# Kernel optimization log

Measured on AMD Instinct MI355X. Metric: run time of the kernel, lower is better.

Reference implementation:

```python
import jax, jax.numpy as jnp
import numpy as np

N_NODES = 50000
N_EDGES = 800000
D = 64
E_DIM = 2
C = 8


def _spline_basis(pseudo, K):
    """Open B-spline basis, degree=1. pseudo: [Ne, E] in [0,1).
    Returns basis B [Ne, S] and flat weight index WI [Ne, S], S = 2**E."""
    E = pseudo.shape[1]
    v = pseudo * (K - 1)
    lo_f = jnp.floor(v)
    frac = v - lo_f
    lo = lo_f.astype(jnp.int32)
    idx = jnp.stack([jnp.clip(lo, 0, K - 1), jnp.clip(lo + 1, 0, K - 1)], axis=-1)  # [Ne,E,2]
    bas = jnp.stack([1.0 - frac, frac], axis=-1)                                   # [Ne,E,2]
    combos = jnp.asarray(
        np.stack(np.meshgrid(*([np.arange(2)] * E), indexing='ij'), -1).reshape(-1, E)
    )  # [S,E]
    d_idx = jnp.arange(E)[None, :]          # broadcast to [S,E]
    B = jnp.prod(bas[:, d_idx, combos], axis=-1)  # [Ne,S]
    stride = (K ** jnp.arange(E)).astype(jnp.int32)  # [E]
    WI = jnp.sum(idx[:, d_idx, combos] * stride[None, None, :], axis=-1)  # [Ne,S]
    return B, WI


def _spline_conv(x, src, dst, pseudo, W, root, bias, K, num_nodes):
    """SplineConv (degree=1, open spline, aggr='mean', root_weight, bias).
    x: [N,Din], W: [K**E, Din, Dout], root: [Din, Dout]."""
    B, WI = _spline_basis(pseudo, K)                 # [Ne,S], [Ne,S]
    Y = jnp.einsum('nd,kdo->nko', x, W)              # [N, K**E, Dout]
    gathered = Y[src[:, None], WI]                   # [Ne, S, Dout]
    m = jnp.einsum('es,eso->eo', B, gathered)        # [Ne, Dout]
    msum = jax.ops.segment_sum(m, dst, num_segments=num_nodes)
    cnt = jax.ops.segment_sum(jnp.ones((m.shape[0], 1), m.dtype), dst, num_segments=num_nodes)
    aggr = msum / jnp.maximum(cnt, 1.0)
    return aggr + x @ root + bias


def setup_inputs() -> dict:
    key = jax.random.key(0)
    ks = jax.random.split(key, 16)
    s = 1.0 / np.sqrt(D)
    return {
        'x': jax.random.normal(ks[0], (N_NODES, D), jnp.float32),
        'edge_index': jax.random.randint(ks[1], (2, N_EDGES), 0, N_NODES, jnp.int32),
        'edge_attr': jax.random.uniform(ks[2], (N_EDGES, E_DIM), jnp.float32),
        'W1': jax.random.normal(ks[3], (3 ** E_DIM, D, D), jnp.float32) * s,
        'root1': jax.random.normal(ks[4], (D, D), jnp.float32) * s,
        'b1': jax.random.normal(ks[5], (D,), jnp.float32) * 0.01,
        'W2': jax.random.normal(ks[6], (5 ** E_DIM, D, D), jnp.float32) * s,
        'root2': jax.random.normal(ks[7], (D, D), jnp.float32) * s,
        'b2': jax.random.normal(ks[8], (D,), jnp.float32) * 0.01,
        'mlp1_w': jax.random.normal(ks[9], (D, D), jnp.float32) * s,
        'mlp1_b': jax.random.normal(ks[10], (D,), jnp.float32) * 0.01,
        'mlp2_w': jax.random.normal(ks[11], (D, C), jnp.float32) * s,
        'mlp2_b': jax.random.normal(ks[12], (C,), jnp.float32) * 0.01,
    }


def reference(x, edge_index, edge_attr, W1, root1, b1, W2, root2, b2,
              mlp1_w, mlp1_b, mlp2_w, mlp2_b):
    N = x.shape[0]
    src, dst = edge_index[0], edge_index[1]
    h = jax.nn.elu(_spline_conv(x, src, dst, edge_attr, W1, root1, b1, 3, N))
    # dropout is identity in eval mode
    h = jax.nn.elu(_spline_conv(h, src, dst, edge_attr, W2, root2, b2, 5, N))
    # task='node', G=0 -> no pooling / no concat
    h = jax.nn.relu(h @ mlp1_w + mlp1_b)
    h = jax.nn.relu(h @ mlp2_w + mlp2_b)
    return h
```

## Files before the change

kernel.cpp:

```cpp
#include <hip/hip_runtime.h>
#include <hip/hip_bf16.h>

typedef __attribute__((ext_vector_type(8))) short short8;
typedef __attribute__((ext_vector_type(4))) short short4v;
typedef __attribute__((ext_vector_type(4))) unsigned int uint4v;
typedef __attribute__((ext_vector_type(4))) float floatx4;
typedef __attribute__((ext_vector_type(16))) float floatx16;

__device__ __forceinline__ unsigned short f2bf(float x) {
  __hip_bfloat16 h = __float2bfloat16(x);
  return __builtin_bit_cast(unsigned short, h);
}
__device__ __forceinline__ float bf2f(unsigned short u) {
  return __builtin_bit_cast(float, (unsigned int)u << 16);
}
__device__ __forceinline__ unsigned int pk_bf16(float lo, float hi) {
  return ((unsigned int)f2bf(hi) << 16) | (unsigned int)f2bf(lo);
}

__device__ __forceinline__ void pack_b_dev(
    const float* __restrict__ W, const float* __restrict__ root,
    unsigned short* __restrict__ Bpk, int K2, int i) {
  int j = i & 7;
  int lane = (i >> 3) & 63;
  int rest = i >> 9;
  int wv = rest & 3, kc = rest >> 2;
  int o = wv * 16 + (lane & 15);
  int p = kc * 32 + ((lane >> 4) & 3) * 8 + j;
  int k = p >> 6, q6 = p & 63;
  float v = (k < K2) ? W[(k << 12) + (q6 << 6) + o] : root[(q6 << 6) + o];
  Bpk[i] = f2bf(v);
}

__global__ __launch_bounds__(256) void prep_kernel(
    const float* __restrict__ W1, const float* __restrict__ root1,
    unsigned short* __restrict__ Bpk1,
    const float* __restrict__ W2, const float* __restrict__ root2,
    unsigned short* __restrict__ Bpk2,
    const float* __restrict__ m1w, unsigned short* __restrict__ m1pk,
    const float4* __restrict__ X, unsigned short* __restrict__ Xbf,
    int* __restrict__ deg, int N) {
  int nbZ = (N + 255) >> 8;
  int b = blockIdx.x, t = threadIdx.x;
  if (b < nbZ) {
    int i = b * 256 + t;
    if (i < N) deg[i] = 0;
    return;
  }
  b -= nbZ;
  if (b < 160) {
    pack_b_dev(W1, root1, Bpk1, 9, b * 256 + t);
    return;
  }
  b -= 160;
  if (b < 416) {
    pack_b_dev(W2, root2, Bpk2, 25, b * 256 + t);
    return;
  }
  b -= 416;
  if (b < 16) {
    pack_b_dev(m1w, m1w, m1pk, 0, b * 256 + t);
    return;
  }
  b -= 16;
  {
    int i = b * 256 + t;
    if (i < N * 16) {
      float4 v = X[i];
      short4v o = {(short)f2bf(v.x), (short)f2bf(v.y),
                   (short)f2bf(v.z), (short)f2bf(v.w)};
      *(short4v*)&Xbf[i * 4] = o;
    }
  }
}

__global__ __launch_bounds__(256) void hist_kernel(
    const int* __restrict__ dst, int* __restrict__ deg, int nE) {
  int e = blockIdx.x * 256 + threadIdx.x;
  if (e < nE) atomicAdd(&deg[dst[e]], 1);
}

__global__ __launch_bounds__(256) void blocksum_kernel(
    const int* __restrict__ deg, int* __restrict__ partial, int N) {
  __shared__ int s[256];
  int t = threadIdx.x, i = blockIdx.x * 256 + t;
  s[t] = (i < N) ? deg[i] : 0;
  __syncthreads();
  for (int off = 128; off > 0; off >>= 1) {
    if (t < off) s[t] += s[t + off];
    __syncthreads();
  }
  if (t == 0) partial[blockIdx.x] = s[0];
}

__global__ __launch_bounds__(256) void blockscan_kernel(
    const int* __restrict__ deg, const int* __restrict__ partial,
    int* __restrict__ row_start, int* __restrict__ cursor,
    int N, int nE, int nb) {
  __shared__ int sp[256];
  __shared__ int s[256];
  __shared__ int base;
  int t = threadIdx.x, i = blockIdx.x * 256 + t;
  int pv = (t < nb) ? partial[t] : 0;
  sp[t] = pv;
  __syncthreads();
  for (int off = 1; off < 256; off <<= 1) {
    int x = (t >= off) ? sp[t - off] : 0;
    __syncthreads();
    sp[t] += x;
    __syncthreads();
  }
  if (t == blockIdx.x) base = sp[t] - pv;
  __syncthreads();
  int v = (i < N) ? deg[i] : 0;
  s[t] = v;
  __syncthreads();
  for (int off = 1; off < 256; off <<= 1) {
    int x = (t >= off) ? s[t - off] : 0;
    __syncthreads();
    s[t] += x;
    __syncthreads();
  }
  if (i < N) {
    int excl = s[t] - v + base;
    row_start[i] = excl;
    cursor[i] = excl;
  }
  if (i == 0) row_start[N] = nE;
}

__global__ __launch_bounds__(256) void scatter_rec_kernel(
    const int* __restrict__ dst, const int* __restrict__ src,
    const float* __restrict__ attr, int* __restrict__ cursor,
    float4* __restrict__ recS, int nE) {
  int e = blockIdx.x * 256 + threadIdx.x;
  if (e < 32) recS[nE + e] = make_float4(0.f, 0.f, 0.f, 0.f);
  if (e >= nE) return;
  int pos = atomicAdd(&cursor[dst[e]], 1);
  float2 a = *(const float2*)&attr[2 * e];
  recS[pos] = make_float4(a.x * 4.f, a.y * 4.f,
                          __builtin_bit_cast(float, src[e] * 64), 0.f);
}

template <int K, int K2, int OUTBF, int NODES, int GRP, int MINW, int PF>
__global__ __launch_bounds__(256, MINW) void spline_layer_kernel(
    const float4* __restrict__ rec, const int* __restrict__ row_start,
    const unsigned short* __restrict__ Xbf, const unsigned short* __restrict__ Bpk,
    const float* __restrict__ bias, void* __restrict__ outv, int N, float uscale) {
  constexpr int RZ = K2 * 64;
  constexpr int AS = RZ + 8;
  constexpr int NKZ = RZ / 32;
  constexpr int NKC = (K2 + 1) * 2;
  __shared__ unsigned short As[NODES * AS];
  __shared__ __align__(16) float invs[16];
  __shared__ int wcur;
  const int t = threadIdx.x, w = t >> 6, lane = t & 63;
  const int nodeBase = blockIdx.x * NODES;

  const int col = lane & 31, half = lane >> 5, col2 = col * 2;
  const float mi0f = (col < K2) ? (float)(col % K) : -1e9f;
  const float mi1f = (col < K2) ? (float)(col / K) : 0.f;

  if (t == 0) wcur = 0;
  if constexpr (NODES < 16) {
    if (w == 3 && lane >= 48 + NODES) invs[lane - 48] = 1.0f;
  }
  __syncthreads();

  int row;
  if (lane == 0) row = atomicAdd(&wcur, 1);
  row = __shfl(row, 0);
  while (row < NODES) {
    const int node = nodeBase + row;
    if (node < N) {
      floatx16 d0, d1;
#pragma unroll
      for (int i = 0; i < 16; ++i) { d0[i] = 0.f; d1[i] = 0.f; }

      const int beg = row_start[node], end = row_start[node + 1];
      if (lane == 0) invs[row] = 1.f / (float)max(end - beg, 1);

      float4 rjn[8];
      if constexpr (PF) {
        const int ib0 = beg + half * 8;
#pragma unroll
        for (int j = 0; j < 8; ++j) rjn[j] = rec[ib0 + j];
      }
      for (int c0 = beg; c0 < end; c0 += 16) {
        float4 rj[8];
        if constexpr (PF) {
#pragma unroll
          for (int j = 0; j < 8; ++j) rj[j] = rjn[j];
        } else {
          const int ib = c0 + half * 8;
#pragma unroll
          for (int j = 0; j < 8; ++j) rj[j] = rec[ib + j];
        }
        unsigned int xv[8];
#pragma unroll
        for (int j = 0; j < 8; ++j)
          xv[j] = *(const unsigned int*)(Xbf +
                    (__builtin_bit_cast(int, rj[j].z) + col2));
        if constexpr (PF) {
          const int ibn = c0 + 16 + half * 8;
#pragma unroll
          for (int j = 0; j < 8; ++j) rjn[j] = rec[ibn + j];
        }
        short8 A;
        const bool fullc = (end - c0 >= 16);
        const int rem = end - (c0 + half * 8);
#pragma unroll
        for (int j = 0; j < 8; ++j) {
          float t0 = fmaf(rj[j].x, -uscale, mi0f);
          float t1 = fmaf(rj[j].y, -uscale, mi1f);
          float su = fmaxf(0.f, 1.f - fabsf(t0));
          float sv = fmaxf(0.f, 1.f - fabsf(t1));
          float p = su * sv;
          if (!fullc) p = (j < rem) ? p : 0.f;
          A[j] = (short)f2bf(p);
        }
        uint4v blo, bhi;
#pragma unroll
        for (int i = 0; i < 4; ++i) {
          blo[i] = __builtin_amdgcn_perm(xv[2 * i + 1], xv[2 * i], 0x05040100u);
          bhi[i] = __builtin_amdgcn_perm(xv[2 * i + 1], xv[2 * i], 0x07060302u);
        }
        d0 = __builtin_amdgcn_mfma_f32_32x32x16_bf16(
                 A, __builtin_bit_cast(short8, blo), d0, 0, 0, 0);
        d1 = __builtin_amdgcn_mfma_f32_32x32x16_bf16(
                 A, __builtin_bit_cast(short8, bhi), d1, 0, 0, 0);
      }

#pragma unroll
      for (int reg = 0; reg < 16; ++reg) {
        int r = (reg & 3) + 8 * (reg >> 2) + 4 * half;
        if (r < K2)
          *(unsigned int*)&As[row * AS + r * 64 + col2] =
              pk_bf16(d0[reg], d1[reg]);
      }
    } else {
      if (lane == 0) invs[row] = 1.0f;
      for (int i = lane; i < RZ / 2; i += 64)
        ((unsigned int*)&As[row * AS])[i] = 0;
    }
    if (lane == 0) row = atomicAdd(&wcur, 1);
    row = __shfl(row, 0);
  }
  __syncthreads();

  const int mrow = lane & 15, q = lane >> 4;
  const int arow = (NODES < 16) ? min(mrow, NODES - 1) : mrow;
  const int anode = min(nodeBase + arow, N - 1);
  floatx4 aZ0 = {0.f, 0.f, 0.f, 0.f};
  floatx4 aZ1 = {0.f, 0.f, 0.f, 0.f};
  floatx4 aR  = {0.f, 0.f, 0.f, 0.f};
#pragma unroll
  for (int kc0 = 0; kc0 < NKC; kc0 += GRP) {
    short8 av[GRP], bv[GRP];
#pragma unroll
    for (int u = 0; u < GRP; ++u) {
      const int kc = kc0 + u;
      if (kc < NKZ)
        av[u] = *(const short8*)&As[arow * AS + kc * 32 + q * 8];
      else
        av[u] = *(const short8*)&Xbf[(size_t)anode * 64 + (kc - NKZ) * 32 + q * 8];
      bv[u] = *(const short8*)&Bpk[(((size_t)kc * 4 + w) * 64 + lane) * 8];
    }
#pragma unroll
    for (int u = 0; u < GRP; ++u) {
      const int kc = kc0 + u;
      if (kc >= NKZ)
        aR = __builtin_amdgcn_mfma_f32_16x16x32_bf16(av[u], bv[u], aR, 0, 0, 0);
      else if ((kc0 / GRP) & 1)
        aZ1 = __builtin_amdgcn_mfma_f32_16x16x32_bf16(av[u], bv[u], aZ1, 0, 0, 0);
      else
        aZ0 = __builtin_amdgcn_mfma_f32_16x16x32_bf16(av[u], bv[u], aZ0, 0, 0, 0);
    }
  }

  const int o = w * 16 + mrow;
  const float bvs = bias[o];
  const floatx4 invv = *(const floatx4*)&invs[q * 4];
#pragma unroll
  for (int reg = 0; reg < 4; ++reg) {
    int rloc = q * 4 + reg;
    int node = nodeBase + rloc;
    if (rloc < NODES && node < N) {
      float v = (aZ0[reg] + aZ1[reg]) * invv[reg] + aR[reg] + bvs;
      v = v > 0.f ? v : (expf(v) - 1.f);
      if (OUTBF)
        ((unsigned short*)outv)[(size_t)node * 64 + o] = f2bf(v);
      else
        ((float*)outv)[(size_t)node * 64 + o] = v;
    }
  }
}

__global__ __launch_bounds__(256) void head_kernel(
    const unsigned short* __restrict__ h2bf, const unsigned short* __restrict__ m1pk,
    const float* __restrict__ m1b, const float* __restrict__ m2w,
    const float* __restrict__ m2b, float* __restrict__ out, int N) {
  __shared__ unsigned short Hs[64 * 72];
  __shared__ unsigned short Ts[64 * 72];
  __shared__ float W2s[512];
  const int t = threadIdx.x, w = t >> 6, lane = t & 63;
  const int n0 = blockIdx.x * 64;

  for (int i = t; i < 512; i += 256) {
    int row = i >> 3, cg = i & 7;
    int n = n0 + row;
    floatx4 val = {0.f, 0.f, 0.f, 0.f};
    if (n < N) val = *(const floatx4*)&h2bf[(size_t)n * 64 + cg * 8];
    *(floatx4*)&Hs[row * 72 + cg * 8] = val;
  }
  for (int i = t; i < 512; i += 256) W2s[i] = m2w[i];
  __syncthreads();

  const int mrow = lane & 15, q = lane >> 4;
  const int o = w * 16 + mrow;
  const float bv = m1b[o];
#pragma unroll
  for (int rg = 0; rg < 4; ++rg) {
    floatx4 acc = {0.f, 0.f, 0.f, 0.f};
#pragma unroll
    for (int kc = 0; kc < 2; ++kc) {
      short8 a = *(const short8*)&Hs[(rg * 16 + mrow) * 72 + kc * 32 + q * 8];
      short8 b = *(const short8*)&m1pk[(((size_t)kc * 4 + w) * 64 + lane) * 8];
      acc = __builtin_amdgcn_mfma_f32_16x16x32_bf16(a, b, acc, 0, 0, 0);
    }
#pragma unroll
    for (int reg = 0; reg < 4; ++reg) {
      int row = rg * 16 + q * 4 + reg;
      float v = acc[reg] + bv;
      Ts[row * 72 + o] = f2bf(v > 0.f ? v : 0.f);
    }
  }
  __syncthreads();

  for (int i = t; i < 512; i += 256) {
    int nl = i >> 3, c = i & 7;
    int n = n0 + nl;
    if (n >= N) continue;
    float s = m2b[c];
    for (int d = 0; d < 64; ++d) s += bf2f(Ts[nl * 72 + d]) * W2s[d * 8 + c];
    out[(size_t)n * 8 + c] = s > 0.f ? s : 0.f;
  }
}

extern "C" void kernel_launch(void* const* d_in, const int* in_sizes, int n_in,
                              void* d_out, int out_size, void* d_ws, size_t ws_size,
                              hipStream_t stream) {
  const float* x     = (const float*)d_in[0];
  const int*   ei    = (const int*)d_in[1];
  const float* attr  = (const float*)d_in[2];
  const float* W1    = (const float*)d_in[3];
  const float* root1 = (const float*)d_in[4];
  const float* b1    = (const float*)d_in[5];
  const float* W2    = (const float*)d_in[6];
  const float* root2 = (const float*)d_in[7];
  const float* b2    = (const float*)d_in[8];
  const float* m1w   = (const float*)d_in[9];
  const float* m1b   = (const float*)d_in[10];
  const float* m2w   = (const float*)d_in[11];
  const float* m2b   = (const float*)d_in[12];

  const int N  = in_sizes[0] / 64;
  const int nE = in_sizes[1] / 2;
  const int* src  = ei;
  const int* dstv = ei + nE;
  float* out = (float*)d_out;

  int* deg       = (int*)d_ws;
  int* row_start = deg + N;
  int* cursor    = row_start + (N + 1);
  int* partial   = cursor + N;
  char* pbase = (char*)(partial + 256);
  pbase = (char*)(((uintptr_t)pbase + 15) & ~(uintptr_t)15);
  float4* recS = (float4*)pbase;
  unsigned short* Xbf  = (unsigned short*)(recS + nE + 32);
  unsigned short* h1bf = Xbf + (size_t)N * 64;
  unsigned short* h2bf = h1bf + (size_t)N * 64;
  unsigned short* Bpk1 = h2bf + (size_t)N * 64;
  unsigned short* Bpk2 = Bpk1 + 64 * 640;
  unsigned short* m1pk = Bpk2 + 64 * 1664;

  dim3 blk(256);
  int nbN  = (N + 255) / 256;
  int nbE  = (nE + 255) / 256;
  int nbF1 = (N + 15) / 16;
  int nbF2 = (N + 9) / 10;
  int nbH  = (N + 63) / 64;
  int nbP  = nbN + 160 + 416 + 16 + (N * 16 + 255) / 256;

  prep_kernel<<<nbP, blk, 0, stream>>>(W1, root1, Bpk1, W2, root2, Bpk2,
                                       m1w, m1pk, (const float4*)x, Xbf,
                                       deg, N);

  hist_kernel<<<nbE, blk, 0, stream>>>(dstv, deg, nE);
  blocksum_kernel<<<nbN, blk, 0, stream>>>(deg, partial, N);
  blockscan_kernel<<<nbN, blk, 0, stream>>>(deg, partial, row_start, cursor,
                                            N, nE, nbN);
  scatter_rec_kernel<<<nbE, blk, 0, stream>>>(dstv, src, attr, cursor, recS, nE);

  spline_layer_kernel<3, 9, 1, 16, 4, 4, 0><<<nbF1, blk, 0, stream>>>(
      recS, row_start, Xbf, Bpk1, b1, h1bf, N, 0.5f);

  spline_layer_kernel<5, 25, 1, 10, 4, 4, 1><<<nbF2, blk, 0, stream>>>(
      recS, row_start, h1bf, Bpk2, b2, h2bf, N, 1.0f);

  head_kernel<<<nbH, blk, 0, stream>>>(h2bf, m1pk, m1b, m2w, m2b, out, N);
}
```

Baseline: 309.6 us.

## Fuse MLP head into second spline layer epilogue

Folds the head MLP (64x64 MFMA plus ReLU, then the 64x8 projection) into the epilogue of the second spline layer. The layer-2 activations now go to shared memory instead of a global bf16 buffer, which drops the h2 round trip and one kernel launch. Nodes per block for layer 2 rise from 10 to 12. The epilogue reuses the As shared buffer and adds extra barriers, and blocks with fewer than 16 nodes leave some MMA rows as unused padding.

```diff
diff --git a/kernel.cpp b/kernel.cpp
--- a/kernel.cpp
+++ b/kernel.cpp
@@ -142,11 +142,13 @@
                           __builtin_bit_cast(float, src[e] * 64), 0.f);
 }
 
-template <int K, int K2, int OUTBF, int NODES, int GRP, int MINW, int PF>
+template <int K, int K2, int OUTBF, int NODES, int GRP, int MINW, int PF, int HEAD>
 __global__ __launch_bounds__(256, MINW) void spline_layer_kernel(
     const float4* __restrict__ rec, const int* __restrict__ row_start,
     const unsigned short* __restrict__ Xbf, const unsigned short* __restrict__ Bpk,
-    const float* __restrict__ bias, void* __restrict__ outv, int N, float uscale) {
+    const float* __restrict__ bias, void* __restrict__ outv, int N, float uscale,
+    const unsigned short* __restrict__ m1pk_g, const float* __restrict__ m1b_g,
+    const float* __restrict__ m2w_g, const float* __restrict__ m2b_g) {
   constexpr int RZ = K2 * 64;
   constexpr int AS = RZ + 8;
   constexpr int NKZ = RZ / 32;
@@ -281,69 +283,61 @@
   const int o = w * 16 + mrow;
   const float bvs = bias[o];
   const floatx4 invv = *(const floatx4*)&invs[q * 4];
-#pragma unroll
-  for (int reg = 0; reg < 4; ++reg) {
-    int rloc = q * 4 + reg;
-    int node = nodeBase + rloc;
-    if (rloc < NODES && node < N) {
-      float v = (aZ0[reg] + aZ1[reg]) * invv[reg] + aR[reg] + bvs;
-      v = v > 0.f ? v : (expf(v) - 1.f);
-      if (OUTBF)
-        ((unsigned short*)outv)[(size_t)node * 64 + o] = f2bf(v);
-      else
-        ((float*)outv)[(size_t)node * 64 + o] = v;
-    }
-  }
-}
-
-__global__ __launch_bounds__(256) void head_kernel(
-    const unsigned short* __restrict__ h2bf, const unsigned short* __restrict__ m1pk,
-    const float* __restrict__ m1b, const float* __restrict__ m2w,
-    const float* __restrict__ m2b, float* __restrict__ out, int N) {
-  __shared__ unsigned short Hs[64 * 72];
-  __shared__ unsigned short Ts[64 * 72];
-  __shared__ float W2s[512];
-  const int t = threadIdx.x, w = t >> 6, lane = t & 63;
-  const int n0 = blockIdx.x * 64;
-
-  for (int i = t; i < 512; i += 256) {
-    int row = i >> 3, cg = i & 7;
-    int n = n0 + row;
-    floatx4 val = {0.f, 0.f, 0.f, 0.f};
-    if (n < N) val = *(const floatx4*)&h2bf[(size_t)n * 64 + cg * 8];
-    *(floatx4*)&Hs[row * 72 + cg * 8] = val;
-  }
-  for (int i = t; i < 512; i += 256) W2s[i] = m2w[i];
-  __syncthreads();
-
-  const int mrow = lane & 15, q = lane >> 4;
-  const int o = w * 16 + mrow;
-  const float bv = m1b[o];
-#pragma unroll
-  for (int rg = 0; rg < 4; ++rg) {
-    floatx4 acc = {0.f, 0.f, 0.f, 0.f};
+
+  if constexpr (HEAD) {
+    __syncthreads();
+    unsigned short* Hs = As;
+    unsigned short* Ts = As + 2048;
+    float* W2s = (float*)(As + 4096);
+    for (int i = t; i < 512; i += 256) W2s[i] = m2w_g[i];
+#pragma unroll
+    for (int reg = 0; reg < 4; ++reg) {
+      int rloc = q * 4 + reg;
+      int node = nodeBase + rloc;
+      if (rloc < NODES && node < N) {
+        float v = (aZ0[reg] + aZ1[reg]) * invv[reg] + aR[reg] + bvs;
+        v = v > 0.f ? v : (expf(v) - 1.f);
+        Hs[rloc * 72 + o] = f2bf(v);
+      }
+    }
+    __syncthreads();
+    floatx4 accT = {0.f, 0.f, 0.f, 0.f};
 #pragma unroll
     for (int kc = 0; kc < 2; ++kc) {
-      short8 a = *(const short8*)&Hs[(rg * 16 + mrow) * 72 + kc * 32 + q * 8];
-      short8 b = *(const short8*)&m1pk[(((size_t)kc * 4 + w) * 64 + lane) * 8];
-      acc = __builtin_amdgcn_mfma_f32_16x16x32_bf16(a, b, acc, 0, 0, 0);
-    }
+      short8 a = *(const short8*)&Hs[arow * 72 + kc * 32 + q * 8];
+      short8 b = *(const short8*)&m1pk_g[(((size_t)kc * 4 + w) * 64 + lane) * 8];
+      accT = __builtin_amdgcn_mfma_f32_16x16x32_bf16(a, b, accT, 0, 0, 0);
+    }
+    const float bT = m1b_g[o];
 #pragma unroll
     for (int reg = 0; reg < 4; ++reg) {
-      int row = rg * 16 + q * 4 + reg;
-      float v = acc[reg] + bv;
-      Ts[row * 72 + o] = f2bf(v > 0.f ? v : 0.f);
-    }
-  }
-  __syncthreads();
-
-  for (int i = t; i < 512; i += 256) {
-    int nl = i >> 3, c = i & 7;
-    int n = n0 + nl;
-    if (n >= N) continue;
-    float s = m2b[c];
-    for (int d = 0; d < 64; ++d) s += bf2f(Ts[nl * 72 + d]) * W2s[d * 8 + c];
-    out[(size_t)n * 8 + c] = s > 0.f ? s : 0.f;
+      float v = accT[reg] + bT;
+      Ts[(q * 4 + reg) * 72 + o] = f2bf(v > 0.f ? v : 0.f);
+    }
+    __syncthreads();
+    if (t < NODES * 8) {
+      int nl = t >> 3, c = t & 7;
+      int node = nodeBase + nl;
+      if (node < N) {
+        float s = m2b_g[c];
+        for (int d = 0; d < 64; ++d) s += bf2f(Ts[nl * 72 + d]) * W2s[d * 8 + c];
+        ((float*)outv)[(size_t)node * 8 + c] = s > 0.f ? s : 0.f;
+      }
+    }
+  } else {
+#pragma unroll
+    for (int reg = 0; reg < 4; ++reg) {
+      int rloc = q * 4 + reg;
+      int node = nodeBase + rloc;
+      if (rloc < NODES && node < N) {
+        float v = (aZ0[reg] + aZ1[reg]) * invv[reg] + aR[reg] + bvs;
+        v = v > 0.f ? v : (expf(v) - 1.f);
+        if (OUTBF)
+          ((unsigned short*)outv)[(size_t)node * 64 + o] = f2bf(v);
+        else
+          ((float*)outv)[(size_t)node * 64 + o] = v;
+      }
+    }
   }
 }
 
@@ -379,8 +373,7 @@
   float4* recS = (float4*)pbase;
   unsigned short* Xbf  = (unsigned short*)(recS + nE + 32);
   unsigned short* h1bf = Xbf + (size_t)N * 64;
-  unsigned short* h2bf = h1bf + (size_t)N * 64;
-  unsigned short* Bpk1 = h2bf + (size_t)N * 64;
+  unsigned short* Bpk1 = h1bf + (size_t)N * 64;
   unsigned short* Bpk2 = Bpk1 + 64 * 640;
   unsigned short* m1pk = Bpk2 + 64 * 1664;
 
@@ -388,8 +381,7 @@
   int nbN  = (N + 255) / 256;
   int nbE  = (nE + 255) / 256;
   int nbF1 = (N + 15) / 16;
-  int nbF2 = (N + 9) / 10;
-  int nbH  = (N + 63) / 64;
+  int nbF2 = (N + 11) / 12;
   int nbP  = nbN + 160 + 416 + 16 + (N * 16 + 255) / 256;
 
   prep_kernel<<<nbP, blk, 0, stream>>>(W1, root1, Bpk1, W2, root2, Bpk2,
@@ -402,11 +394,11 @@
                                             N, nE, nbN);
   scatter_rec_kernel<<<nbE, blk, 0, stream>>>(dstv, src, attr, cursor, recS, nE);
 
-  spline_layer_kernel<3, 9, 1, 16, 4, 4, 0><<<nbF1, blk, 0, stream>>>(
-      recS, row_start, Xbf, Bpk1, b1, h1bf, N, 0.5f);
-
-  spline_layer_kernel<5, 25, 1, 10, 4, 4, 1><<<nbF2, blk, 0, stream>>>(
-      recS, row_start, h1bf, Bpk2, b2, h2bf, N, 1.0f);
-
-  head_kernel<<<nbH, blk, 0, stream>>>(h2bf, m1pk, m1b, m2w, m2b, out, N);
-}
+  spline_layer_kernel<3, 9, 1, 16, 4, 4, 0, 0><<<nbF1, blk, 0, stream>>>(
+      recS, row_start, Xbf, Bpk1, b1, h1bf, N, 0.5f,
+      m1pk, m1b, m2w, m2b);
+
+  spline_layer_kernel<5, 25, 0, 12, 4, 4, 1, 1><<<nbF2, blk, 0, stream>>>(
+      recS, row_start, h1bf, Bpk2, b2, out, N, 1.0f,
+      m1pk, m1b, m2w, m2b);
+}
```

New measurement: 298.9 us. 1.04x faster.
